# Performance work log

Hardware: AMD Instinct MI355X
Metric: run time of the kernel (lower is better)

The kernel has to match this reference:

```python
import jax, jax.numpy as jnp
import numpy as np

DIM = 3000  # featureDim hard-coded in the module
BANDS = [(0, 122), (122, 244), (244, 366), (366, 488), (488, 972)]


def _make_basis(dim, start, end):
    # np.fft.rfft(eye(dim)) -> (dim, dim//2+1); zero columns outside [start, end]
    fb = np.fft.rfft(np.eye(dim))
    mask = np.zeros(dim // 2 + 1)
    mask[start:end + 1] = 1.0
    return jnp.asarray((fb * mask).astype(np.complex64))


def setup_inputs() -> dict:
    key = jax.random.key(0)
    k1, k2, k3 = jax.random.split(key, 3)
    B, C_in, C_out, K = 8, 64, 128, 25
    signal = jax.random.normal(k1, (B, C_in, DIM), dtype=jnp.float32)
    weight = jax.random.normal(k2, (C_out, C_in, K), dtype=jnp.float32)
    bias = jax.random.normal(k3, (C_out,), dtype=jnp.float32)
    fbs = [_make_basis(DIM, s, e) for (s, e) in BANDS]
    return {
        "signal": signal, "weight": weight, "bias": bias,
        "fb1": fbs[0], "fb2": fbs[1], "fb3": fbs[2], "fb4": fbs[3], "fb5": fbs[4],
    }


def reference(signal, weight, bias, fb1, fb2, fb3, fb4, fb5):
    # signal: [B, C_in, L] with L == DIM (padding=0, L even -> no extra pads)
    # weight: [C_out, C_in, K]; dilation=1 so kron/cutoff is a no-op
    B, C_in, L = signal.shape
    C_out, _, K = weight.shape

    # zero-pad kernel to length L and take (conjugated) rfft, as in the torch code
    padded_kernel = jnp.pad(weight, ((0, 0), (0, 0), (0, L - K)))
    kfr = jnp.conj(jnp.fft.rfft(padded_kernel, axis=-1))  # [C_out, C_in, L//2+1]

    sig_c = signal.astype(jnp.complex64)

    q = C_out // 5
    band_slices = [(0, q), (q, 2 * q), (2 * q, 3 * q), (3 * q, 4 * q), (4 * q, C_out)]
    bases = [fb1, fb2, fb3, fb4, fb5]

    outs = []
    for fb, (lo, hi) in zip(bases, band_slices):
        sig_fr = jnp.matmul(sig_c, fb)                    # [B, C_in, F] banded DFT
        # groups=1 complex matmul over input channels, per frequency
        outs.append(jnp.einsum('bif,oif->bof', sig_fr, kfr[lo:hi]))
    out_fr = jnp.concatenate(outs, axis=1)                # [B, C_out, F]

    out = jnp.fft.irfft(out_fr, axis=-1)                  # [B, C_out, L]
    out = out[:, :, : L - K + 1]                          # valid crop, stride=1
    out = out + bias[None, :, None]
    return out
```

## Files before the change

kernel.cpp:

```cpp
#include <hip/hip_runtime.h>

#define L_SIG 3000
#define KPAD2 1536
#define NB 8
#define CIN 64
#define COUT 128
#define KW 25
#define TOUT 2976
#define FMAXB 973
#define PSTRIDE2 (2048 * 512)
#define NTT 1536

#define AE_BYTE   0
#define AO_BYTE   1572864
#define BC_BYTE   3145728
#define BS_BYTE   6291456
#define TC_BYTE   9437184
#define TS_BYTE   12582912
#define WC_BYTE   15728640
#define SP_BYTE   22544384
#define AR_BYTE   31457280
#define AI_BYTE   31981568

typedef _Float16 f16x8 __attribute__((ext_vector_type(8)));
typedef float f32x4 __attribute__((ext_vector_type(4)));

typedef __attribute__((address_space(1))) const unsigned GU;
typedef __attribute__((address_space(3))) unsigned LU;
#define GL16(g, l) __builtin_amdgcn_global_load_lds((GU*)(g), (LU*)(l), 16, 0, 0)

#define TWO_PI_OVER_L 0.00209439510239319549f

__device__ __forceinline__ float2 h2f2(unsigned u) {
    union { unsigned u; _Float16 h[2]; } p; p.u = u;
    return make_float2((float)p.h[0], (float)p.h[1]);
}
__device__ __forceinline__ unsigned f2h2(float a, float b) {
    union { unsigned u; _Float16 h[2]; } p;
    p.h[0] = (_Float16)a; p.h[1] = (_Float16)b; return p.u;
}

__global__ __launch_bounds__(256) void k_prep(const float* __restrict__ sig,
                                              const float* __restrict__ w,
                                              char* __restrict__ wsb) {
    __shared__ float wL[CIN * KW];
    const int startv[5] = {0,122,244,366,488};
    const int binsv[5]  = {123,123,123,123,485};
    int blk = blockIdx.x, tid = threadIdx.x;

    if (blk < 512) {
        const float* x = sig + (size_t)blk * L_SIG;
        _Float16* AE = (_Float16*)(wsb + AE_BYTE);
        _Float16* AO = (_Float16*)(wsb + AO_BYTE);
        for (int g2 = tid; g2 < 384; g2 += 256) {
            int half = (g2 >= 192);
            int g = g2 - (half ? 192 : 0);
            union { _Float16 h[8]; uint4 u; } p;
            p.u = make_uint4(0, 0, 0, 0);
            if (g < 188) {
                int k0 = g * 8;
                float4 f0 = *(const float4*)(x + k0);
                float4 f1 = *(const float4*)(x + k0 + 4);
                float4 m0 = *(const float4*)(x + 2992 - k0);
                float4 m1 = *(const float4*)(x + 2996 - k0);
                float mir0 = k0 ? x[3000 - k0] : 0.f;
                float fwd[8]  = {f0.x,f0.y,f0.z,f0.w,f1.x,f1.y,f1.z,f1.w};
                float span[8] = {m0.x,m0.y,m0.z,m0.w,m1.x,m1.y,m1.z,m1.w};
                #pragma unroll
                for (int j = 0; j < 8; ++j) {
                    int k = k0 + j;
                    float mv = (j == 0) ? mir0 : span[8 - j];
                    float xe, xo;
                    if (k == 0)         { xe = fwd[0];      xo = 0.f; }
                    else if (k < 1500)  { xe = fwd[j] + mv; xo = fwd[j] - mv; }
                    else if (k == 1500) { xe = fwd[j];      xo = 0.f; }
                    else                { xe = 0.f;         xo = 0.f; }
                    p.h[j] = (_Float16)(half ? xo : xe);
                }
            }
            int gsw = (g & ~7) | ((g & 7) ^ (blk & 7));
            ((uint4*)(half ? AO : AE))[(size_t)blk * 192 + gsw] = p.u;
        }

    } else if (blk < 2560) {
        int q = blk - 512;
        int isin = (q >= 1024);
        int f = q & 1023;
        _Float16* Bm = (_Float16*)(wsb + (isin ? BS_BYTE : BC_BYTE));
        int g = tid;
        if (g >= 192) return;
        union { _Float16 h[8]; uint4 u; } p;
        p.u = make_uint4(0, 0, 0, 0);
        if (f < FMAXB) {
            int k0 = g * 8;
            int m0 = (int)(((long long)f * k0) % 3000);
            float s0, c0, sw, cw;
            __sincosf((float)m0 * TWO_PI_OVER_L, &s0, &c0);
            __sincosf((float)f * TWO_PI_OVER_L, &sw, &cw);
            float rr = c0, ri = -s0;
            #pragma unroll
            for (int j = 0; j < 8; ++j) {
                p.h[j] = (_Float16)(isin ? ri : rr);
                float nr = rr * cw + ri * sw;
                float ni = ri * cw - rr * sw;
                rr = nr; ri = ni;
            }
        }
        int gsw = (g & ~7) | ((g & 7) ^ (f & 7));
        ((uint4*)Bm)[(size_t)f * 192 + gsw] = p.u;

    } else if (blk < 4096) {
        const int tb4[5] = {0, 24576, 49152, 73728, 98304};
        int t = blk - 2560;
        int m = tid >> 7;
        int gi = tid & 127;
        int band, g;
        if (gi < 64) { band = gi >> 4; g = gi & 15; }
        else         { band = 4;       g = gi - 64; }
        int Kb8 = (band < 4) ? 16 : 64;
        int bins = binsv[band];
        int fl0 = g * 8;
        int f0 = startv[band] + fl0;
        union { _Float16 h[8]; uint4 u; } p;
        p.u = make_uint4(0, 0, 0, 0);
        int m0 = (f0 * t) % 3000;
        float s0, c0, sw, cw;
        __sincosf((float)m0 * TWO_PI_OVER_L, &s0, &c0);
        __sincosf((float)t * TWO_PI_OVER_L, &sw, &cw);
        float rr = c0, ri = -s0;
        #pragma unroll
        for (int j = 0; j < 8; ++j) {
            if (fl0 + j < bins) p.h[j] = (_Float16)(m ? ri : rr);
            float nr = rr * cw + ri * sw;
            float ni = ri * cw - rr * sw;
            rr = nr; ri = ni;
        }
        uint4* Tm = (uint4*)(wsb + (m ? TS_BYTE : TC_BYTE));
        Tm[(size_t)tb4[band] + (size_t)t * Kb8 + g] = p.u;

    } else if (blk < 4352) {
        _Float16* Wc = (_Float16*)(wsb + WC_BYTE);
        const int n_ov[5]   = {25,25,25,25,28};
        const size_t wbase[5] = {0, 393600, 787200, 1180800, 1574400};
        int q = blk - 4096;
        int o = q >> 1;
        int f = (q & 1) * 256 + tid;
        int band = min(o / 25, 4);
        int o_local = o - band * 25;
        int bins = binsv[band];
        const float* wrow = w + (size_t)o * CIN * KW;
        for (int k = tid; k < CIN * KW; k += 256) wL[k] = wrow[k];
        __syncthreads();
        if (f >= bins) return;
        int n_o = n_ov[band];
        int fg = startv[band] + f;
        float ws_, wc_;
        __sincosf((float)fg * TWO_PI_OVER_L, &ws_, &wc_);
        float wr = wc_, wi = ws_;
        unsigned* outp = (unsigned*)Wc + (wbase[band] >> 1) + ((size_t)f * n_o + o_local) * 64;
        for (int i = 0; i < CIN; ++i) {
            float ar = 0.f, ai = 0.f;
            float rr = 1.0f, ri = 0.0f;
            const float* wv = wL + i * KW;
            #pragma unroll
            for (int t = 0; t < KW; ++t) {
                float x = wv[t];
                ar = fmaf(x, rr, ar);
                ai = fmaf(x, ri, ai);
                float nr = fmaf(-ri, wi, rr * wr);
                float ni = fmaf( ri, wr, rr * wi);
                rr = nr; ri = ni;
            }
            outp[i] = f2h2(ar, ai);
        }

    } else {
        uint4* Az = (uint4*)(wsb + AR_BYTE);
        int q = blk - 4352;
        Az[(size_t)q * 256 + tid] = make_uint4(0, 0, 0, 0);
    }
}

__global__ __launch_bounds__(256) void k_dft_mm(const char* __restrict__ wsb,
                                                float* __restrict__ Sp) {
    __shared__ _Float16 As[2][64 * 128];
    __shared__ _Float16 Bs[2][64 * 128];
    int z = blockIdx.z;
    const _Float16* A = (const _Float16*)(wsb + (z ? AO_BYTE : AE_BYTE));
    const _Float16* B = (const _Float16*)(wsb + (z ? BS_BYTE : BC_BYTE));
    int row0 = (blockIdx.y & 7) * 64;
    int kh   = blockIdx.y >> 3;
    int col0 = blockIdx.x * 64;
    int kt0  = kh * 6;
    const int nkt = 6;
    int tid = threadIdx.x, wid = tid >> 6, lane = tid & 63;
    int wr = wid >> 1, wc = wid & 1;
    f32x4 acc[2][2] = {};

    auto stage = [&](int kt, int buf) {
        int k0g = (kt0 + kt) * 16;
        #pragma unroll
        for (int it = 0; it < 4; ++it) {
            int cb = it * 256 + wid * 64;
            int c = cb + lane;
            int ar = c >> 4, cir = c & 15;
            GL16((const char*)A + ((size_t)(row0 + ar) * 192 + k0g + cir) * 16,
                 (char*)As[buf] + cb * 16);
            GL16((const char*)B + ((size_t)(col0 + ar) * 192 + k0g + cir) * 16,
                 (char*)Bs[buf] + cb * 16);
        }
    };
    stage(0, 0);
    for (int kt = 0; kt < nkt; ++kt) {
        int cur = kt & 1;
        asm volatile("s_waitcnt vmcnt(0)" ::: "memory");
        __syncthreads();
        if (kt + 1 < nkt) stage(kt + 1, cur ^ 1);
        #pragma unroll
        for (int ks = 0; ks < 4; ++ks) {
            f16x8 av[2], bv[2];
            #pragma unroll
            for (int m = 0; m < 2; ++m) {
                int r = wr * 32 + m * 16 + (lane & 15);
                int gq = ks * 4 + (lane >> 4);
                int g = (gq & ~7) | ((gq & 7) ^ (r & 7));
                av[m] = *(const f16x8*)(As[cur] + r * 128 + g * 8);
            }
            #pragma unroll
            for (int n = 0; n < 2; ++n) {
                int r = wc * 32 + n * 16 + (lane & 15);
                int gq = ks * 4 + (lane >> 4);
                int g = (gq & ~7) | ((gq & 7) ^ (r & 7));
                bv[n] = *(const f16x8*)(Bs[cur] + r * 128 + g * 8);
            }
            #pragma unroll
            for (int m = 0; m < 2; ++m)
                #pragma unroll
                for (int n = 0; n < 2; ++n)
                    acc[m][n] = __builtin_amdgcn_mfma_f32_16x16x32_f16(
                        av[m], bv[n], acc[m][n], 0, 0, 0);
        }
    }
    float* outp = Sp + (size_t)kh * PSTRIDE2;
    #pragma unroll
    for (int m = 0; m < 2; ++m)
        #pragma unroll
        for (int n = 0; n < 2; ++n) {
            int colf = col0 + wc * 32 + n * 16 + (lane & 15);
            int scol = 2 * colf + z;
            int rowb = row0 + wr * 32 + m * 16 + (lane >> 4) * 4;
            *(float4*)(outp + (size_t)scol * 512 + rowb) = *(float4*)&acc[m][n];
        }
}

__global__ __launch_bounds__(256) void k_mix(const float* __restrict__ Sp,
                                             const _Float16* __restrict__ Wc,
                                             char* __restrict__ wsb) {
    __shared__ float s_re[8 * 72];
    __shared__ float s_im[8 * 72];
    const int startv[5] = {0,122,244,366,488};
    const int n_ov[5]   = {25,25,25,25,28};
    const int kbv[5]    = {128,128,128,128,512};
    const size_t wbase[5] = {0, 393600, 787200, 1180800, 1574400};
    const size_t arbase[5] = {0, 32768, 65536, 98304, 131072};
    const int cumb[6] = {0, 123, 246, 369, 492, 977};
    int blk = blockIdx.x, tid = threadIdx.x;
    int band = 0;
    while (blk >= cumb[band + 1]) band++;
    int f_local = blk - cumb[band];
    int fg = startv[band] + f_local;

    const float* p0 = Sp + (size_t)(2 * fg) * 512;
    const float* p1 = p0 + (size_t)PSTRIDE2;
    #pragma unroll
    for (int e = 0; e < 2; ++e) {
        int row = tid + e * 256;
        int b = row >> 6, i = row & 63;
        s_re[b * 72 + i] = p0[row] + p1[row];
        s_im[b * 72 + i] = p0[512 + row] + p1[512 + row];
    }
    __syncthreads();

    int o_local = tid >> 3, b = tid & 7;
    int n_o = n_ov[band];
    if (o_local >= n_o) return;
    const uint4* wp4 = (const uint4*)((const unsigned*)Wc + (wbase[band] >> 1) +
                                      ((size_t)f_local * n_o + o_local) * 64);
    const float* lre = s_re + b * 72;
    const float* lim = s_im + b * 72;
    float xr = 0.f, xi = 0.f;
    #pragma unroll
    for (int ii = 0; ii < 16; ++ii) {
        float4 r4 = *(const float4*)(lre + ii * 4);
        float4 i4 = *(const float4*)(lim + ii * 4);
        uint4 wq = wp4[ii];
        float2 wv;
        wv = h2f2(wq.x);
        xr = fmaf(r4.x, wv.x, xr); xr = fmaf(-i4.x, wv.y, xr);
        xi = fmaf(r4.x, wv.y, xi); xi = fmaf( i4.x, wv.x, xi);
        wv = h2f2(wq.y);
        xr = fmaf(r4.y, wv.x, xr); xr = fmaf(-i4.y, wv.y, xr);
        xi = fmaf(r4.y, wv.y, xi); xi = fmaf( i4.y, wv.x, xi);
        wv = h2f2(wq.z);
        xr = fmaf(r4.z, wv.x, xr); xr = fmaf(-i4.z, wv.y, xr);
        xi = fmaf(r4.z, wv.y, xi); xi = fmaf( i4.z, wv.x, xi);
        wv = h2f2(wq.w);
        xr = fmaf(r4.w, wv.x, xr); xr = fmaf(-i4.w, wv.y, xr);
        xi = fmaf(r4.w, wv.y, xi); xi = fmaf( i4.w, wv.x, xi);
    }
    float scale = (fg == 0 ? 1.0f : 2.0f) / 3000.0f;
    size_t ha = arbase[band] + (size_t)(o_local * 8 + b) * kbv[band] + f_local;
    ((_Float16*)(wsb + AR_BYTE))[ha] = (_Float16)(xr * scale);
    ((_Float16*)(wsb + AI_BYTE))[ha] = (_Float16)(xi * scale);
}

__global__ __launch_bounds__(256) void k_idft_mm(const char* __restrict__ wsb,
                                                 const float* __restrict__ bias,
                                                 float* __restrict__ out) {
    __shared__ _Float16 AsR[2][4096];
    __shared__ _Float16 AsI[2][4096];
    __shared__ _Float16 BsC[2][4096];
    __shared__ _Float16 BsS[2][4096];
    const int n_ov[5] = {25,25,25,25,28};
    const int kbv[5]  = {128,128,128,128,512};
    const size_t arbase[5] = {0, 32768, 65536, 98304, 131072};
    const size_t tbase[5]  = {0, 196608, 393216, 589824, 786432};
    int mt = blockIdx.y;
    int band = mt >> 2;
    int row0b = (mt & 3) * 64;
    int col0 = blockIdx.x * 64;
    int Kb = kbv[band];
    int nkt = Kb / 64;
    const char* Ar_b = wsb + AR_BYTE + arbase[band] * 2;
    const char* Ai_b = wsb + AI_BYTE + arbase[band] * 2;
    const char* Tc_b = wsb + TC_BYTE + tbase[band] * 2;
    const char* Ts_b = wsb + TS_BYTE + tbase[band] * 2;
    int tid = threadIdx.x, wid = tid >> 6, lane = tid & 63;
    int wr = wid >> 1, wc = wid & 1;
    f32x4 accE[2][2] = {};
    f32x4 accO[2][2] = {};

    auto stage = [&](int kt, int buf) {
        int k0 = kt * 64;
        #pragma unroll
        for (int it = 0; it < 2; ++it) {
            int cb = it * 256 + wid * 64;
            int c = cb + lane;
            int ar = c >> 3, cir = c & 7;
            int cirs = cir ^ (ar & 7);
            size_t aoff = ((size_t)(row0b + ar) * Kb + k0) * 2 + cirs * 16;
            size_t boff = ((size_t)(col0 + ar) * Kb + k0) * 2 + cirs * 16;
            GL16(Ar_b + aoff, (char*)AsR[buf] + cb * 16);
            GL16(Ai_b + aoff, (char*)AsI[buf] + cb * 16);
            GL16(Tc_b + boff, (char*)BsC[buf] + cb * 16);
            GL16(Ts_b + boff, (char*)BsS[buf] + cb * 16);
        }
    };
    stage(0, 0);
    for (int kt = 0; kt < nkt; ++kt) {
        int cur = kt & 1;
        asm volatile("s_waitcnt vmcnt(0)" ::: "memory");
        __syncthreads();
        if (kt + 1 < nkt) stage(kt + 1, cur ^ 1);
        #pragma unroll
        for (int ks = 0; ks < 2; ++ks) {
            f16x8 avR[2], avI[2], bvC[2], bvS[2];
            #pragma unroll
            for (int m = 0; m < 2; ++m) {
                int r = wr * 32 + m * 16 + (lane & 15);
                int g = (ks * 4 + (lane >> 4)) ^ (r & 7);
                avR[m] = *(const f16x8*)(AsR[cur] + r * 64 + g * 8);
                avI[m] = *(const f16x8*)(AsI[cur] + r * 64 + g * 8);
            }
            #pragma unroll
            for (int n = 0; n < 2; ++n) {
                int r = wc * 32 + n * 16 + (lane & 15);
                int g = (ks * 4 + (lane >> 4)) ^ (r & 7);
                bvC[n] = *(const f16x8*)(BsC[cur] + r * 64 + g * 8);
                bvS[n] = *(const f16x8*)(BsS[cur] + r * 64 + g * 8);
            }
            #pragma unroll
            for (int m = 0; m < 2; ++m)
                #pragma unroll
                for (int n = 0; n < 2; ++n) {
                    accE[m][n] = __builtin_amdgcn_mfma_f32_16x16x32_f16(
                        avR[m], bvC[n], accE[m][n], 0, 0, 0);
                    accO[m][n] = __builtin_amdgcn_mfma_f32_16x16x32_f16(
                        avI[m], bvS[n], accO[m][n], 0, 0, 0);
                }
        }
    }

    int n_o8 = n_ov[band] * 8;
    #pragma unroll
    for (int m = 0; m < 2; ++m)
        #pragma unroll
        for (int n = 0; n < 2; ++n) {
            int t = col0 + wc * 32 + n * 16 + (lane & 15);
            int rowb = row0b + wr * 32 + m * 16 + (lane >> 4) * 4;
            #pragma unroll
            for (int j = 0; j < 4; ++j) {
                int prb = rowb + j;
                if (prb < n_o8) {
                    int o = band * 25 + (prb >> 3);
                    int b = prb & 7;
                    float E = accE[m][n][j], O = accO[m][n][j];
                    float bv = bias[o];
                    size_t rb = ((size_t)b * COUT + o) * TOUT;
                    if (t <= 1500)
                        out[rb + t] = E + O + bv;
                    if (t >= 25 && t <= 1499)
                        out[rb + 3000 - t] = E - O + bv;
                }
            }
        }
}

extern "C" void kernel_launch(void* const* d_in, const int* in_sizes, int n_in,
                              void* d_out, int out_size, void* d_ws, size_t ws_size,
                              hipStream_t stream) {
    const float* sig  = (const float*)d_in[0];
    const float* w    = (const float*)d_in[1];
    const float* bias = (const float*)d_in[2];
    float* out = (float*)d_out;
    char* wsb = (char*)d_ws;
    _Float16* Wc  = (_Float16*)(wsb + WC_BYTE);
    float*    Sp  = (float*)(wsb + SP_BYTE);

    k_prep   <<<dim3(4608),      256, 0, stream>>>(sig, w, wsb);
    k_dft_mm <<<dim3(16, 16, 2), 256, 0, stream>>>(wsb, Sp);
    k_mix    <<<dim3(977),       256, 0, stream>>>(Sp, Wc, wsb);
    k_idft_mm<<<dim3(24, 20),    256, 0, stream>>>(wsb, bias, out);
}
```

Measured before the change: 68.18 us.

## Rebalance kernel-FFT work, drop split-K in DFT matmul, schedule heavy band first

The weight-spectrum precompute in k_prep now assigns 64 frequencies per block and splits the 64 input channels across four thread groups, giving more blocks and shorter serial loops (band 5 gets 8 chunks). The DFT matmul drops its 2-way split-K, so each block runs all 12 k-tiles and writes Sp directly, and k_mix no longer sums two partial buffers. The inverse-DFT launch maps the first row tiles to the heavy band 4 (K=512) so the long blocks start first. This trades fewer dft_mm blocks (less parallelism) for removing the partial-sum traffic and the extra adds.

```diff
diff --git a/kernel.cpp b/kernel.cpp
--- a/kernel.cpp
+++ b/kernel.cpp
@@ -8,7 +8,6 @@
 #define KW 25
 #define TOUT 2976
 #define FMAXB 973
-#define PSTRIDE2 (2048 * 512)
 #define NTT 1536
 
 #define AE_BYTE   0
@@ -138,19 +137,22 @@
         uint4* Tm = (uint4*)(wsb + (m ? TS_BYTE : TC_BYTE));
         Tm[(size_t)tb4[band] + (size_t)t * Kb8 + g] = p.u;
 
-    } else if (blk < 4352) {
+    } else if (blk < 4520) {
         _Float16* Wc = (_Float16*)(wsb + WC_BYTE);
         const int n_ov[5]   = {25,25,25,25,28};
         const size_t wbase[5] = {0, 393600, 787200, 1180800, 1574400};
         int q = blk - 4096;
-        int o = q >> 1;
-        int f = (q & 1) * 256 + tid;
+        int o, fchunk;
+        if (q < 200) { o = q >> 1; fchunk = q & 1; }
+        else { int q2 = q - 200; o = 100 + (q2 >> 3); fchunk = q2 & 7; }
         int band = min(o / 25, 4);
         int o_local = o - band * 25;
         int bins = binsv[band];
         const float* wrow = w + (size_t)o * CIN * KW;
         for (int k = tid; k < CIN * KW; k += 256) wL[k] = wrow[k];
         __syncthreads();
+        int fl = tid & 63, iq = tid >> 6;
+        int f = fchunk * 64 + fl;
         if (f >= bins) return;
         int n_o = n_ov[band];
         int fg = startv[band] + f;
@@ -158,7 +160,8 @@
         __sincosf((float)fg * TWO_PI_OVER_L, &ws_, &wc_);
         float wr = wc_, wi = ws_;
         unsigned* outp = (unsigned*)Wc + (wbase[band] >> 1) + ((size_t)f * n_o + o_local) * 64;
-        for (int i = 0; i < CIN; ++i) {
+        #pragma unroll 4
+        for (int i = iq * 16; i < iq * 16 + 16; ++i) {
             float ar = 0.f, ai = 0.f;
             float rr = 1.0f, ri = 0.0f;
             const float* wv = wL + i * KW;
@@ -176,7 +179,7 @@
 
     } else {
         uint4* Az = (uint4*)(wsb + AR_BYTE);
-        int q = blk - 4352;
+        int q = blk - 4520;
         Az[(size_t)q * 256 + tid] = make_uint4(0, 0, 0, 0);
     }
 }
@@ -188,17 +191,15 @@
     int z = blockIdx.z;
     const _Float16* A = (const _Float16*)(wsb + (z ? AO_BYTE : AE_BYTE));
     const _Float16* B = (const _Float16*)(wsb + (z ? BS_BYTE : BC_BYTE));
-    int row0 = (blockIdx.y & 7) * 64;
-    int kh   = blockIdx.y >> 3;
+    int row0 = blockIdx.y * 64;
     int col0 = blockIdx.x * 64;
-    int kt0  = kh * 6;
-    const int nkt = 6;
+    const int nkt = 12;
     int tid = threadIdx.x, wid = tid >> 6, lane = tid & 63;
     int wr = wid >> 1, wc = wid & 1;
     f32x4 acc[2][2] = {};
 
     auto stage = [&](int kt, int buf) {
-        int k0g = (kt0 + kt) * 16;
+        int k0g = kt * 16;
         #pragma unroll
         for (int it = 0; it < 4; ++it) {
             int cb = it * 256 + wid * 64;
@@ -241,7 +242,6 @@
                         av[m], bv[n], acc[m][n], 0, 0, 0);
         }
     }
-    float* outp = Sp + (size_t)kh * PSTRIDE2;
     #pragma unroll
     for (int m = 0; m < 2; ++m)
         #pragma unroll
@@ -249,7 +249,7 @@
             int colf = col0 + wc * 32 + n * 16 + (lane & 15);
             int scol = 2 * colf + z;
             int rowb = row0 + wr * 32 + m * 16 + (lane >> 4) * 4;
-            *(float4*)(outp + (size_t)scol * 512 + rowb) = *(float4*)&acc[m][n];
+            *(float4*)(Sp + (size_t)scol * 512 + rowb) = *(float4*)&acc[m][n];
         }
 }
 
@@ -271,13 +271,12 @@
     int fg = startv[band] + f_local;
 
     const float* p0 = Sp + (size_t)(2 * fg) * 512;
-    const float* p1 = p0 + (size_t)PSTRIDE2;
     #pragma unroll
     for (int e = 0; e < 2; ++e) {
         int row = tid + e * 256;
         int b = row >> 6, i = row & 63;
-        s_re[b * 72 + i] = p0[row] + p1[row];
-        s_im[b * 72 + i] = p0[512 + row] + p1[512 + row];
+        s_re[b * 72 + i] = p0[row];
+        s_im[b * 72 + i] = p0[512 + row];
     }
     __syncthreads();
 
@@ -326,8 +325,9 @@
     const size_t arbase[5] = {0, 32768, 65536, 98304, 131072};
     const size_t tbase[5]  = {0, 196608, 393216, 589824, 786432};
     int mt = blockIdx.y;
-    int band = mt >> 2;
-    int row0b = (mt & 3) * 64;
+    int band, row0b;
+    if (mt < 4) { band = 4;            row0b = mt * 64; }
+    else        { band = (mt - 4) >> 2; row0b = ((mt - 4) & 3) * 64; }
     int col0 = blockIdx.x * 64;
     int Kb = kbv[band];
     int nkt = Kb / 64;
@@ -427,8 +427,8 @@
     _Float16* Wc  = (_Float16*)(wsb + WC_BYTE);
     float*    Sp  = (float*)(wsb + SP_BYTE);
 
-    k_prep   <<<dim3(4608),      256, 0, stream>>>(sig, w, wsb);
-    k_dft_mm <<<dim3(16, 16, 2), 256, 0, stream>>>(wsb, Sp);
-    k_mix    <<<dim3(977),       256, 0, stream>>>(Sp, Wc, wsb);
-    k_idft_mm<<<dim3(24, 20),    256, 0, stream>>>(wsb, bias, out);
-}
+    k_prep   <<<dim3(4776),     256, 0, stream>>>(sig, w, wsb);
+    k_dft_mm <<<dim3(16, 8, 2), 256, 0, stream>>>(wsb, Sp);
+    k_mix    <<<dim3(977),      256, 0, stream>>>(Sp, Wc, wsb);
+    k_idft_mm<<<dim3(24, 20),   256, 0, stream>>>(wsb, bias, out);
+}
```

New measurement: 57.57 us, median of 2. 1.18x faster.
